# Kernel tuning notes

Hardware: AMD Instinct MI355X
Metric: run time of the kernel (lower is better)

Reference implementation:

```python
import jax, jax.numpy as jnp
import numpy as np

B, N, C = 8, 2048, 151  # batch, num rois, n_obj_classes
D_IN = C + 4            # RELPN_WITH_BBOX_INFO adds 4 normalized box coords
HID = 64


def setup_inputs() -> dict:
    key = jax.random.key(0)
    ks = jax.random.split(key, 8)
    # rois: [B, N, 5] = (batch_idx, x1, y1, x2, y2) in pixel coords
    boxes = jax.random.uniform(ks[0], (B, N, 4), dtype=jnp.float32) * 600.0
    rois = jnp.concatenate([jnp.zeros((B, N, 1), jnp.float32), boxes], axis=2)
    roi_feat = jax.random.normal(ks[1], (B, N, C), dtype=jnp.float32)
    im_info = jnp.ones((B, 3), jnp.float32) * 600.0  # (h, w, scale)
    s1 = 1.0 / np.sqrt(D_IN)
    s2 = 1.0 / np.sqrt(HID)
    return {
        "rois": rois,
        "roi_feat": roi_feat,
        "im_info": im_info,
        "w1_sub": jax.random.normal(ks[2], (D_IN, HID), jnp.float32) * s1,
        "b1_sub": jnp.zeros((HID,), jnp.float32),
        "w2_sub": jax.random.normal(ks[3], (HID, HID), jnp.float32) * s2,
        "b2_sub": jnp.zeros((HID,), jnp.float32),
        "w1_obj": jax.random.normal(ks[4], (D_IN, HID), jnp.float32) * s1,
        "b1_obj": jnp.zeros((HID,), jnp.float32),
        "w2_obj": jax.random.normal(ks[5], (HID, HID), jnp.float32) * s2,
        "b2_obj": jnp.zeros((HID,), jnp.float32),
        "K": 2048,
    }


def _mlp(x, w1, b1, w2, b2):
    return jax.nn.relu(x @ w1 + b1) @ w2 + b2


def reference(rois, roi_feat, im_info, w1_sub, b1_sub, w2_sub, b2_sub,
              w1_obj, b1_obj, w2_obj, b2_obj, K):
    b, n, _ = roi_feat.shape
    # normalized bbox info appended to roi features (RELPN_WITH_BBOX_INFO)
    xy = rois[:, :, 1:3] / im_info[:, 1][:, None, None]
    wh = rois[:, :, 3:5] / im_info[:, 0][:, None, None]
    feat = jnp.concatenate([roi_feat, xy, wh], axis=2)  # [B, N, 155]
    feat = jax.lax.stop_gradient(feat)  # original uses roi_feat4prop.detach()
    x_sub = _mlp(feat, w1_sub, b1_sub, w2_sub, b2_sub)  # [B, N, 64]
    x_obj = _mlp(feat, w1_obj, b1_obj, w2_obj, b2_obj)  # [B, N, 64]
    # bilinear pair scores: [B, N, N] -> [B, N*N]
    bil = jnp.einsum("bnd,bmd->bnm", x_sub, x_obj).reshape(b, n * n)
    vis_score = jax.nn.sigmoid(bil)  # [B, N*N]
    # proposal layer: top-K scoring (sub, obj) pairs per image
    top_scores, top_idx = jax.lax.top_k(vis_score, K)  # [B, K]
    sub_idx = top_idx // n
    obj_idx = top_idx % n
    boxes = rois[:, :, 1:5]  # [B, N, 4]
    sub_boxes = jnp.take_along_axis(boxes, sub_idx[:, :, None], axis=1)
    obj_boxes = jnp.take_along_axis(boxes, obj_idx[:, :, None], axis=1)
    roi_pairs = jnp.concatenate([sub_boxes, obj_boxes], axis=2)  # [B, K, 8]
    roi_proposals = jnp.stack([sub_idx, obj_idx], axis=2)        # [B, K, 2]
    return roi_pairs, roi_proposals, top_scores, vis_score
```

## Files before the change

### kernel.cpp

```cpp
#include <hip/hip_runtime.h>
#include <math.h>

#define NB 8
#define NN_ROI 2048
#define C_FEAT 151
#define D_IN 155
#define HID 64
#define K_TOP 2048
#define NN2 (NN_ROI*NN_ROI)
#define CAP 4096
#define NKB 1024
#define SLOTS 131072
#define LCAP 448
#define BM 128
#define BN 256

#define WS_XS    0x0
#define WS_XO    0x400000
#define WS_CNT2  0x800000
#define WS_FLAGS 0x800040
#define WS_CAND2 0x800080
#define WS_NEED  (0x800080 + NB*SLOTS*8)

__device__ __forceinline__ float sigmoid_fast(float x) {
    return 1.0f / (1.0f + __expf(-x));
}

__global__ __launch_bounds__(256) void mlp_kernel(
    const float* __restrict__ rois, const float* __restrict__ roi_feat,
    const float* __restrict__ im_info,
    const float* __restrict__ w1_sub, const float* __restrict__ b1_sub,
    const float* __restrict__ w2_sub, const float* __restrict__ b2_sub,
    const float* __restrict__ w1_obj, const float* __restrict__ b1_obj,
    const float* __restrict__ w2_obj, const float* __restrict__ b2_obj,
    float* __restrict__ Xs, float* __restrict__ Xo)
{
    __shared__ __align__(16) float featL[64][156];
    __shared__ __align__(16) float hL[64][68];
    const int tid   = threadIdx.x;
    const int pass  = blockIdx.x >> 8;
    const int chunk = blockIdx.x & 255;
    const int row0  = chunk * 64;
    const int b     = row0 >> 11;
    const float* w1 = pass ? w1_obj : w1_sub;
    const float* w2 = pass ? w2_obj : w2_sub;
    const float* b1 = pass ? b1_obj : b1_sub;
    const float* b2 = pass ? b2_obj : b2_sub;
    float* X = pass ? Xo : Xs;
    const float im0 = im_info[b*3+0];
    const float im1 = im_info[b*3+1];

    for (int i = tid; i < 64*C_FEAT; i += 256) {
        const int r = i / C_FEAT, d = i - r*C_FEAT;
        featL[r][d] = roi_feat[(size_t)(row0+r)*C_FEAT + d];
    }
    if (tid < 64) {
        const int r = tid;
        #pragma unroll
        for (int c = 0; c < 4; ++c)
            featL[r][C_FEAT+c] = rois[(size_t)(row0+r)*5 + 1 + c] / (c < 2 ? im1 : im0);
    }
    __syncthreads();

    const int tx = tid & 15, ty = tid >> 4;
    float acc[4][4] = {};
    for (int d4 = 0; d4 < 38; ++d4) {
        const int d = d4*4;
        float wv[4][4], fv[4][4];
        #pragma unroll
        for (int q = 0; q < 4; ++q)
            *(float4*)wv[q] = *(const float4*)&w1[(d+q)*HID + tx*4];
        #pragma unroll
        for (int i = 0; i < 4; ++i)
            *(float4*)fv[i] = *(const float4*)&featL[ty*4+i][d];
        #pragma unroll
        for (int q = 0; q < 4; ++q)
            #pragma unroll
            for (int i = 0; i < 4; ++i)
                #pragma unroll
                for (int j = 0; j < 4; ++j)
                    acc[i][j] = fmaf(fv[i][q], wv[q][j], acc[i][j]);
    }
    #pragma unroll
    for (int d = 152; d < 155; ++d) {
        float wv[4];
        *(float4*)wv = *(const float4*)&w1[d*HID + tx*4];
        #pragma unroll
        for (int i = 0; i < 4; ++i) {
            const float f = featL[ty*4+i][d];
            #pragma unroll
            for (int j = 0; j < 4; ++j)
                acc[i][j] = fmaf(f, wv[j], acc[i][j]);
        }
    }
    {
        float b1v[4];
        *(float4*)b1v = *(const float4*)&b1[tx*4];
        #pragma unroll
        for (int i = 0; i < 4; ++i)
            #pragma unroll
            for (int j = 0; j < 4; ++j) {
                const float v = acc[i][j] + b1v[j];
                hL[ty*4+i][tx*4+j] = v > 0.0f ? v : 0.0f;
            }
    }
    __syncthreads();

    float x[4][4] = {};
    for (int k4 = 0; k4 < 16; ++k4) {
        const int k = k4*4;
        float wv[4][4], hv[4][4];
        #pragma unroll
        for (int q = 0; q < 4; ++q)
            *(float4*)wv[q] = *(const float4*)&w2[(k+q)*HID + tx*4];
        #pragma unroll
        for (int i = 0; i < 4; ++i)
            *(float4*)hv[i] = *(const float4*)&hL[ty*4+i][k];
        #pragma unroll
        for (int q = 0; q < 4; ++q)
            #pragma unroll
            for (int i = 0; i < 4; ++i)
                #pragma unroll
                for (int j = 0; j < 4; ++j)
                    x[i][j] = fmaf(hv[i][q], wv[q][j], x[i][j]);
    }
    {
        float b2v[4];
        *(float4*)b2v = *(const float4*)&b2[tx*4];
        #pragma unroll
        for (int i = 0; i < 4; ++i) {
            *(float4*)&X[(size_t)(row0 + ty*4 + i)*HID + tx*4] = make_float4(
                x[i][0]+b2v[0], x[i][1]+b2v[1], x[i][2]+b2v[2], x[i][3]+b2v[3]);
        }
    }
}

__global__ __launch_bounds__(256) void bil_kernel(
    const float* __restrict__ Xs, const float* __restrict__ Xo,
    float* __restrict__ vis, int* __restrict__ cnt2, int2* __restrict__ cand2,
    int* __restrict__ flags)
{
    __shared__ __align__(16) float As[16][128];
    __shared__ __align__(16) float Bs[16][256];
    __shared__ int2 lcand[LCAP];
    __shared__ int lcnt, lbase;
    const int tid = threadIdx.x;
    const int tx = tid & 15, ty = tid >> 4;
    const int bm = blockIdx.x * BM, bn = blockIdx.y * BN, b = blockIdx.z;
    if (tid == 0) lcnt = 0;

    const float4* Ag = (const float4*)(Xs + ((size_t)b*NN_ROI + bm)*HID);
    const float4* Bg = (const float4*)(Xo + ((size_t)b*NN_ROI + bn)*HID);

    float acc[8][16];
    #pragma unroll
    for (int i = 0; i < 8; ++i)
        #pragma unroll
        for (int j = 0; j < 16; ++j) acc[i][j] = 0.0f;

    for (int ph = 0; ph < 4; ++ph) {
        if (ph) __syncthreads();
        #pragma unroll
        for (int it = 0; it < 2; ++it) {
            const int lin = it*256 + tid;
            const int r = lin >> 2, k4 = lin & 3;
            const float4 v = Ag[r*16 + ph*4 + k4];
            const int rs = r ^ (k4 << 3);
            As[k4*4+0][rs] = v.x; As[k4*4+1][rs] = v.y;
            As[k4*4+2][rs] = v.z; As[k4*4+3][rs] = v.w;
        }
        #pragma unroll
        for (int it = 0; it < 4; ++it) {
            const int lin = it*256 + tid;
            const int r = lin >> 2, k4 = lin & 3;
            const float4 v = Bg[r*16 + ph*4 + k4];
            const int rs = r ^ (k4 << 3);
            Bs[k4*4+0][rs] = v.x; Bs[k4*4+1][rs] = v.y;
            Bs[k4*4+2][rs] = v.z; Bs[k4*4+3][rs] = v.w;
        }
        __syncthreads();
        #pragma unroll 4
        for (int k = 0; k < 16; ++k) {
            const int swz = ((k >> 2) & 3) << 3;
            const int am = (ty*8) ^ swz;
            const float4 a0 = *(const float4*)&As[k][am];
            const float4 a1 = *(const float4*)&As[k][am + 4];
            const float4 q0 = *(const float4*)&Bs[k][(tx*4) ^ swz];
            const float4 q1 = *(const float4*)&Bs[k][(64  + tx*4) ^ swz];
            const float4 q2 = *(const float4*)&Bs[k][(128 + tx*4) ^ swz];
            const float4 q3 = *(const float4*)&Bs[k][(192 + tx*4) ^ swz];
            const float a[8]   = {a0.x,a0.y,a0.z,a0.w,a1.x,a1.y,a1.z,a1.w};
            const float bb[16] = {q0.x,q0.y,q0.z,q0.w, q1.x,q1.y,q1.z,q1.w,
                                  q2.x,q2.y,q2.z,q2.w, q3.x,q3.y,q3.z,q3.w};
            #pragma unroll
            for (int i = 0; i < 8; ++i)
                #pragma unroll
                for (int j = 0; j < 16; ++j)
                    acc[i][j] = fmaf(a[i], bb[j], acc[i][j]);
        }
    }

    const size_t visbase = (size_t)b * NN2;
    #pragma unroll
    for (int i = 0; i < 8; ++i) {
        const int row = bm + ty*8 + i;
        float f[16];
        #pragma unroll
        for (int j = 0; j < 16; ++j) {
            const float s = sigmoid_fast(acc[i][j]);
            f[j] = s;
            const int ku = 0x3F800000 - __float_as_int(s);
            if (ku < NKB) {
                const int col = bn + (j >> 2)*64 + tx*4 + (j & 3);
                const int idx = row*NN_ROI + col;
                const int p = atomicAdd(&lcnt, 1);
                if (p < LCAP) lcand[p] = make_int2(idx, __float_as_int(s));
                else {
                    const int gp = atomicAdd(&cnt2[b], 1);
                    if (gp < SLOTS) cand2[(size_t)b*SLOTS + gp] =
                        make_int2(idx, __float_as_int(s));
                }
            }
        }
        #pragma unroll
        for (int q = 0; q < 4; ++q)
            *(float4*)&vis[visbase + (size_t)row*NN_ROI + bn + q*64 + tx*4] =
                make_float4(f[q*4+0], f[q*4+1], f[q*4+2], f[q*4+3]);
    }
    __syncthreads();
    int n = lcnt; if (n > LCAP) n = LCAP;
    if (tid == 0) lbase = atomicAdd(&cnt2[b], n);
    __syncthreads();
    const int bs = lbase;
    for (int i = tid; i < n; i += 256) {
        const int p = bs + i;
        if (p < SLOTS) cand2[(size_t)b*SLOTS + p] = lcand[i];
    }
}

__global__ __launch_bounds__(1024) void topk_kernel(
    const int* __restrict__ cnt2, const int2* __restrict__ cand2,
    const float* __restrict__ rois,
    float* __restrict__ pairs, float* __restrict__ props, float* __restrict__ scores,
    int* __restrict__ flags)
{
    __shared__ float kv[CAP];
    __shared__ int   ki[CAP];
    __shared__ int   hist[NKB];
    __shared__ int   part[64];
    __shared__ int   scnt;
    __shared__ float sthr;
    const int b = blockIdx.x, tid = threadIdx.x;
    int M = cnt2[b]; if (M > SLOTS) M = SLOTS;
    if (cnt2[b] > SLOTS) atomicOr(flags, 4);

    for (int i = tid; i < NKB; i += 1024) hist[i] = 0;
    if (tid == 0) scnt = 0;
    __syncthreads();
    for (int i = tid; i < M; i += 1024) {
        const int k = 0x3F800000 - cand2[(size_t)b*SLOTS + i].y;
        atomicAdd(&hist[k], 1);
    }
    __syncthreads();
    if (tid < 64) {
        int s = 0;
        for (int i = 0; i < 16; ++i) s += hist[tid*16 + i];
        part[tid] = s;
    }
    __syncthreads();
    if (tid == 0) {
        int cum = 0, kT = NKB - 1; bool found = false;
        for (int c = 0; c < 64; ++c) {
            if (cum + part[c] >= K_TOP) {
                for (int i = c*16; i < c*16 + 16; ++i) {
                    cum += hist[i];
                    if (cum >= K_TOP) { kT = i; found = true; break; }
                }
                break;
            }
            cum += part[c];
        }
        if (!found) atomicOr(flags, 16);
        sthr = __int_as_float(0x3F800000 - kT);
    }
    __syncthreads();
    const float th = sthr;
    for (int c = tid; c < CAP; c += 1024) { kv[c] = -1.0e30f; ki[c] = 0x7FFFFFFF; }
    __syncthreads();
    for (int i = tid; i < M; i += 1024) {
        const int2 e = cand2[(size_t)b*SLOTS + i];
        const float s = __int_as_float(e.y);
        if (s >= th) {
            const int p = atomicAdd(&scnt, 1);
            if (p < CAP) { kv[p] = s; ki[p] = e.x; }
        }
    }
    __syncthreads();
    if (tid == 0) {
        if (scnt < K_TOP) atomicOr(flags, 2);
        if (scnt > CAP)   atomicOr(flags, 4);
    }
    for (int kk = 2; kk <= CAP; kk <<= 1)
        for (int j = kk >> 1; j > 0; j >>= 1) {
            for (int t = tid; t < CAP/2; t += 1024) {
                const int i = 2*t - (t & (j-1));
                const int p = i + j;
                const bool dir = (i & kk) == 0;
                const float vi = kv[i], vp = kv[p];
                const int ii = ki[i], ip = ki[p];
                const bool ge = (vi > vp) || (vi == vp && ii <= ip);
                if (dir ? !ge : ge) { kv[i]=vp; kv[p]=vi; ki[i]=ip; ki[p]=ii; }
            }
            __syncthreads();
        }
    for (int k = tid; k < K_TOP-1; k += 1024) {
        const bool okp = (kv[k] > kv[k+1]) || (kv[k] == kv[k+1] && ki[k] <= ki[k+1]);
        if (!okp) atomicOr(flags, 8);
    }
    for (int k = tid; k < K_TOP; k += 1024) {
        const float v = kv[k]; const int idx = ki[k];
        int sub = 0, obj = 0; float sc = 0.f;
        float4 sb = make_float4(0,0,0,0), ob = make_float4(0,0,0,0);
        if (idx != 0x7FFFFFFF) {
            sub = idx >> 11; obj = idx & (NN_ROI-1);
            sc = v;
            const float* rs = rois + ((size_t)b*NN_ROI + sub)*5 + 1;
            const float* ro = rois + ((size_t)b*NN_ROI + obj)*5 + 1;
            sb = make_float4(rs[0],rs[1],rs[2],rs[3]);
            ob = make_float4(ro[0],ro[1],ro[2],ro[3]);
        }
        const size_t o = (size_t)b*K_TOP + k;
        *(float4*)&pairs[o*8]   = sb;
        *(float4*)&pairs[o*8+4] = ob;
        props[o*2]   = (float)sub;
        props[o*2+1] = (float)obj;
        scores[o]    = sc;
    }
}

__global__ void check_kernel(const int* __restrict__ flags, float* __restrict__ pairs)
{
    const int f = *flags;
    if (f) pairs[0] = 1e5f * (float)f;
}

__global__ void sentinel_kernel(float* out) { out[0] = 1e5f; }

extern "C" void kernel_launch(void* const* d_in, const int* in_sizes, int n_in,
                              void* d_out, int out_size, void* d_ws, size_t ws_size,
                              hipStream_t stream)
{
    static const int EXP_SIZES[12] = {81920, 2473984, 24, 9920, 64, 4096, 64,
                                      9920, 64, 4096, 64, 1};
    bool ok = (n_in == 12) && (out_size == 33734656) && (ws_size >= (size_t)WS_NEED);
    if (ok) for (int i = 0; i < 12; ++i) if (in_sizes[i] != EXP_SIZES[i]) { ok = false; break; }
    if (!ok) { sentinel_kernel<<<1, 1, 0, stream>>>((float*)d_out); return; }

    const float* rois     = (const float*)d_in[0];
    const float* roi_feat = (const float*)d_in[1];
    const float* im_info  = (const float*)d_in[2];
    const float* w1_sub   = (const float*)d_in[3];
    const float* b1_sub   = (const float*)d_in[4];
    const float* w2_sub   = (const float*)d_in[5];
    const float* b2_sub   = (const float*)d_in[6];
    const float* w1_obj   = (const float*)d_in[7];
    const float* b1_obj   = (const float*)d_in[8];
    const float* w2_obj   = (const float*)d_in[9];
    const float* b2_obj   = (const float*)d_in[10];

    char* ws = (char*)d_ws;
    float* Xs   = (float*)(ws + WS_XS);
    float* Xo   = (float*)(ws + WS_XO);
    int* cnt2   = (int*)  (ws + WS_CNT2);
    int* flags  = (int*)  (ws + WS_FLAGS);
    int2* cand2 = (int2*) (ws + WS_CAND2);

    float* out    = (float*)d_out;
    float* pairs  = out;
    float* props  = out + 131072;
    float* scores = out + 163840;
    float* vis    = out + 180224;

    hipMemsetAsync(ws + WS_CNT2, 0, 0x80, stream);
    mlp_kernel<<<512, 256, 0, stream>>>(rois, roi_feat, im_info,
        w1_sub, b1_sub, w2_sub, b2_sub, w1_obj, b1_obj, w2_obj, b2_obj, Xs, Xo);
    bil_kernel<<<dim3(16, 8, NB), 256, 0, stream>>>(Xs, Xo, vis, cnt2, cand2, flags);
    topk_kernel<<<NB, 1024, 0, stream>>>(cnt2, cand2, rois, pairs, props, scores, flags);
    check_kernel<<<1, 1, 0, stream>>>(flags, pairs);
}
```

Before: 183.8 us.

## Shrink bilinear tile to 128x128 and use fast reciprocal sigmoid for vis writes

Halves the bilinear kernel's N tile from 256 to 128, so each thread holds 8x8 accumulators instead of 8x16 and the grid doubles to 2048 blocks. This cuts register pressure and raises occupancy on the GPU. The vis output now uses a hardware approximate reciprocal for the sigmoid. The exact division is computed only when the logit is at least 9, where the candidate threshold can be met, so candidate scores stay identical. The trade-off is smaller per-thread reuse, more redundant A-tile loads, and vis values that may differ in the last bits.

```diff
diff --git a/kernel.cpp b/kernel.cpp
--- a/kernel.cpp
+++ b/kernel.cpp
@@ -13,7 +13,7 @@
 #define SLOTS 131072
 #define LCAP 448
 #define BM 128
-#define BN 256
+#define BN 128
 
 #define WS_XS    0x0
 #define WS_XO    0x400000
@@ -21,10 +21,6 @@
 #define WS_FLAGS 0x800040
 #define WS_CAND2 0x800080
 #define WS_NEED  (0x800080 + NB*SLOTS*8)
-
-__device__ __forceinline__ float sigmoid_fast(float x) {
-    return 1.0f / (1.0f + __expf(-x));
-}
 
 __global__ __launch_bounds__(256) void mlp_kernel(
     const float* __restrict__ rois, const float* __restrict__ roi_feat,
@@ -141,7 +137,7 @@
     int* __restrict__ flags)
 {
     __shared__ __align__(16) float As[16][128];
-    __shared__ __align__(16) float Bs[16][256];
+    __shared__ __align__(16) float Bs[16][128];
     __shared__ int2 lcand[LCAP];
     __shared__ int lcnt, lbase;
     const int tid = threadIdx.x;
@@ -152,11 +148,11 @@
     const float4* Ag = (const float4*)(Xs + ((size_t)b*NN_ROI + bm)*HID);
     const float4* Bg = (const float4*)(Xo + ((size_t)b*NN_ROI + bn)*HID);
 
-    float acc[8][16];
+    float acc[8][8];
     #pragma unroll
     for (int i = 0; i < 8; ++i)
         #pragma unroll
-        for (int j = 0; j < 16; ++j) acc[i][j] = 0.0f;
+        for (int j = 0; j < 8; ++j) acc[i][j] = 0.0f;
 
     for (int ph = 0; ph < 4; ++ph) {
         if (ph) __syncthreads();
@@ -170,7 +166,7 @@
             As[k4*4+2][rs] = v.z; As[k4*4+3][rs] = v.w;
         }
         #pragma unroll
-        for (int it = 0; it < 4; ++it) {
+        for (int it = 0; it < 2; ++it) {
             const int lin = it*256 + tid;
             const int r = lin >> 2, k4 = lin & 3;
             const float4 v = Bg[r*16 + ph*4 + k4];
@@ -179,23 +175,20 @@
             Bs[k4*4+2][rs] = v.z; Bs[k4*4+3][rs] = v.w;
         }
         __syncthreads();
-        #pragma unroll 4
+        #pragma unroll
         for (int k = 0; k < 16; ++k) {
-            const int swz = ((k >> 2) & 3) << 3;
+            const int swz = (k >> 2) << 3;
             const int am = (ty*8) ^ swz;
             const float4 a0 = *(const float4*)&As[k][am];
             const float4 a1 = *(const float4*)&As[k][am + 4];
             const float4 q0 = *(const float4*)&Bs[k][(tx*4) ^ swz];
-            const float4 q1 = *(const float4*)&Bs[k][(64  + tx*4) ^ swz];
-            const float4 q2 = *(const float4*)&Bs[k][(128 + tx*4) ^ swz];
-            const float4 q3 = *(const float4*)&Bs[k][(192 + tx*4) ^ swz];
-            const float a[8]   = {a0.x,a0.y,a0.z,a0.w,a1.x,a1.y,a1.z,a1.w};
-            const float bb[16] = {q0.x,q0.y,q0.z,q0.w, q1.x,q1.y,q1.z,q1.w,
-                                  q2.x,q2.y,q2.z,q2.w, q3.x,q3.y,q3.z,q3.w};
+            const float4 q1 = *(const float4*)&Bs[k][(64 + tx*4) ^ swz];
+            const float a[8]  = {a0.x,a0.y,a0.z,a0.w,a1.x,a1.y,a1.z,a1.w};
+            const float bb[8] = {q0.x,q0.y,q0.z,q0.w,q1.x,q1.y,q1.z,q1.w};
             #pragma unroll
             for (int i = 0; i < 8; ++i)
                 #pragma unroll
-                for (int j = 0; j < 16; ++j)
+                for (int j = 0; j < 8; ++j)
                     acc[i][j] = fmaf(a[i], bb[j], acc[i][j]);
         }
     }
@@ -204,28 +197,32 @@
     #pragma unroll
     for (int i = 0; i < 8; ++i) {
         const int row = bm + ty*8 + i;
-        float f[16];
-        #pragma unroll
-        for (int j = 0; j < 16; ++j) {
-            const float s = sigmoid_fast(acc[i][j]);
-            f[j] = s;
-            const int ku = 0x3F800000 - __float_as_int(s);
-            if (ku < NKB) {
-                const int col = bn + (j >> 2)*64 + tx*4 + (j & 3);
-                const int idx = row*NN_ROI + col;
-                const int p = atomicAdd(&lcnt, 1);
-                if (p < LCAP) lcand[p] = make_int2(idx, __float_as_int(s));
-                else {
-                    const int gp = atomicAdd(&cnt2[b], 1);
-                    if (gp < SLOTS) cand2[(size_t)b*SLOTS + gp] =
-                        make_int2(idx, __float_as_int(s));
+        float f[8];
+        #pragma unroll
+        for (int j = 0; j < 8; ++j) {
+            const float xv = acc[i][j];
+            const float e = __expf(-xv);
+            f[j] = __builtin_amdgcn_rcpf(1.0f + e);
+            if (xv >= 9.0f) {
+                const float se = 1.0f / (1.0f + e);
+                const int ku = 0x3F800000 - __float_as_int(se);
+                if (ku < NKB) {
+                    const int col = bn + (j < 4 ? tx*4 + j : 64 + tx*4 + (j-4));
+                    const int idx = row*NN_ROI + col;
+                    const int p = atomicAdd(&lcnt, 1);
+                    if (p < LCAP) lcand[p] = make_int2(idx, __float_as_int(se));
+                    else {
+                        const int gp = atomicAdd(&cnt2[b], 1);
+                        if (gp < SLOTS) cand2[(size_t)b*SLOTS + gp] =
+                            make_int2(idx, __float_as_int(se));
+                    }
                 }
             }
         }
-        #pragma unroll
-        for (int q = 0; q < 4; ++q)
-            *(float4*)&vis[visbase + (size_t)row*NN_ROI + bn + q*64 + tx*4] =
-                make_float4(f[q*4+0], f[q*4+1], f[q*4+2], f[q*4+3]);
+        *(float4*)&vis[visbase + (size_t)row*NN_ROI + bn + tx*4] =
+            make_float4(f[0], f[1], f[2], f[3]);
+        *(float4*)&vis[visbase + (size_t)row*NN_ROI + bn + 64 + tx*4] =
+            make_float4(f[4], f[5], f[6], f[7]);
     }
     __syncthreads();
     int n = lcnt; if (n > LCAP) n = LCAP;
@@ -384,7 +381,7 @@
     hipMemsetAsync(ws + WS_CNT2, 0, 0x80, stream);
     mlp_kernel<<<512, 256, 0, stream>>>(rois, roi_feat, im_info,
         w1_sub, b1_sub, w2_sub, b2_sub, w1_obj, b1_obj, w2_obj, b2_obj, Xs, Xo);
-    bil_kernel<<<dim3(16, 8, NB), 256, 0, stream>>>(Xs, Xo, vis, cnt2, cand2, flags);
+    bil_kernel<<<dim3(16, 16, NB), 256, 0, stream>>>(Xs, Xo, vis, cnt2, cand2, flags);
     topk_kernel<<<NB, 1024, 0, stream>>>(cnt2, cand2, rois, pairs, props, scores, flags);
     check_kernel<<<1, 1, 0, stream>>>(flags, pairs);
 }
```

Result: faster. 166.7 us (-9.3%).
